# Kernel tuning notes

Measured on AMD Instinct MI355X. Metric: run time of the kernel, lower is better.

Reference implementation:

```python
import jax, jax.numpy as jnp
import numpy as np

IN_FEATURES = 8192
OUT_FEATURES = 8192
BATCH = 64


def setup_inputs() -> dict:
    key = jax.random.key(0)
    k_x, k_mu = jax.random.split(key)
    x = jax.random.normal(k_x, (BATCH, IN_FEATURES), dtype=jnp.float32)
    # torch init: mu = rand(in,1) * out_features; sigma = ones*10; amplitude = ones; bias = zeros
    mu = jax.random.uniform(k_mu, (IN_FEATURES, 1), dtype=jnp.float32) * OUT_FEATURES
    sigma = jnp.ones((IN_FEATURES, 1), dtype=jnp.float32) * 10.0
    amplitude = jnp.ones((IN_FEATURES, 1), dtype=jnp.float32)
    bias = jnp.zeros((OUT_FEATURES,), dtype=jnp.float32)
    return {"x": x, "mu": mu, "sigma": sigma, "amplitude": amplitude, "bias": bias}


def reference(x, mu, sigma, amplitude, bias):
    out_features = bias.shape[0]
    positions = jnp.arange(out_features, dtype=x.dtype)[None, :]  # [1, out]
    diff = positions - mu                                          # [in, out]
    weight = amplitude * jnp.exp(-(diff * diff) / (2.0 * sigma * sigma))  # [in, out]
    out = x @ weight                                               # [B, out]
    return jax.nn.relu(out + bias)
```

## Files before the change

### kernel.cpp

```cpp
#include <hip/hip_runtime.h>

#define IN_F 8192
#define OUT_F 8192
#define BATCH 64
#define TQ 64
#define NTILE (OUT_F / TQ)
#define ROWS 16
#define PASS 2048
#define CH 64

__global__ __launch_bounds__(256) void transpose_x_kern(const float* __restrict__ x,
                                                        float* __restrict__ xT) {
    __shared__ float tile[64][65];
    const int i0 = blockIdx.x * 64;
    const int tid = threadIdx.x;
#pragma unroll
    for (int u = tid; u < 64 * 64; u += 256) {
        const int b = u >> 6;
        const int i = u & 63;
        tile[i][b] = x[b * IN_F + i0 + i];
    }
    __syncthreads();
#pragma unroll
    for (int u = tid; u < 64 * 64; u += 256) {
        const int i = u >> 6;
        const int b = u & 63;
        xT[(i0 + i) * 64 + b] = tile[i][b];
    }
}

__global__ __launch_bounds__(256, 2) void gauss_fc_kern(
    const float* __restrict__ x, const float* __restrict__ xT,
    const float4* __restrict__ mu4, const float4* __restrict__ sg4,
    const float* __restrict__ amp, const float* __restrict__ bias,
    float* __restrict__ out, const int use_xt) {

    __shared__ float4 list[PASS];
    __shared__ float wtile[CH][64];
    __shared__ float xtile[CH][ROWS];
    __shared__ int   cnt;

    const int tid = threadIdx.x;
    const int cc = (tid & 31) << 1;
    const int g = tid >> 5;
    const int g2 = g << 1;
    const int tile0 = blockIdx.x * TQ;
    const int row0 = blockIdx.y * ROWS;
    const float lo = (float)tile0;
    const float hi = (float)(tile0 + TQ - 1);

    float acc00 = 0.f, acc01 = 0.f, acc10 = 0.f, acc11 = 0.f;

    for (int base = 0; base < IN_F; base += PASS) {
        if (tid == 0) cnt = 0;
        __syncthreads();

        const int q_end = (base + PASS) >> 2;
        for (int q = (base >> 2) + tid; q < q_end; q += 256) {
            const float4 m4 = mu4[q];
            const float4 s4 = sg4[q];
            const float ms[4] = {m4.x, m4.y, m4.z, m4.w};
            const float ss[4] = {s4.x, s4.y, s4.z, s4.w};
#pragma unroll
            for (int e = 0; e < 4; ++e) {
                const float m = ms[e];
                const float s = ss[e];
                const float R = 5.0f * fabsf(s) + 1.0f;
                if (m >= lo - R && m <= hi + R) {
                    const int i = (q << 2) + e;
                    const int p = atomicAdd(&cnt, 1);
                    list[p] = make_float4(m, -0.72134752f / (s * s), amp[i],
                                          __int_as_float(i));
                }
            }
        }
        __syncthreads();
        const int n = cnt;

        for (int cb = 0; cb < n; cb += CH) {
            const int cn = min(CH, n - cb);

            for (int u = tid; u < (cn << 6); u += 256) {
                const int j = u >> 6;
                const int col = u & 63;
                const float4 e = list[cb + j];
                const float d = (float)(tile0 + col) - e.x;
                wtile[j][col] = e.z * exp2f(e.y * d * d);
            }
            {
                const int ci = tid >> 2;
                const int rq = (tid & 3) << 2;
                if (ci < cn) {
                    const int i = __float_as_int(list[cb + ci].w);
                    if (use_xt) {
                        *(float4*)&xtile[ci][rq] = *(const float4*)&xT[i * 64 + row0 + rq];
                    } else {
                        xtile[ci][rq + 0] = x[(size_t)(row0 + rq + 0) * IN_F + i];
                        xtile[ci][rq + 1] = x[(size_t)(row0 + rq + 1) * IN_F + i];
                        xtile[ci][rq + 2] = x[(size_t)(row0 + rq + 2) * IN_F + i];
                        xtile[ci][rq + 3] = x[(size_t)(row0 + rq + 3) * IN_F + i];
                    }
                }
            }
            __syncthreads();

#pragma unroll 8
            for (int j = 0; j < cn; ++j) {
                const float2 wv = *(const float2*)&wtile[j][cc];
                const float2 xv = *(const float2*)&xtile[j][g2];
                acc00 += wv.x * xv.x;
                acc01 += wv.x * xv.y;
                acc10 += wv.y * xv.x;
                acc11 += wv.y * xv.y;
            }
            __syncthreads();
        }
    }

    const float b0 = bias[tile0 + cc];
    const float b1 = bias[tile0 + cc + 1];
    const int r0 = row0 + g2;
    float2 v0 = make_float2(fmaxf(acc00 + b0, 0.f), fmaxf(acc10 + b1, 0.f));
    float2 v1 = make_float2(fmaxf(acc01 + b0, 0.f), fmaxf(acc11 + b1, 0.f));
    *(float2*)&out[(size_t)r0 * OUT_F + tile0 + cc]       = v0;
    *(float2*)&out[(size_t)(r0 + 1) * OUT_F + tile0 + cc] = v1;
}

extern "C" void kernel_launch(void* const* d_in, const int* in_sizes, int n_in,
                              void* d_out, int out_size, void* d_ws, size_t ws_size,
                              hipStream_t stream) {
    const float* x     = (const float*)d_in[0];
    const float* mu    = (const float*)d_in[1];
    const float* sigma = (const float*)d_in[2];
    const float* amp   = (const float*)d_in[3];
    const float* bias  = (const float*)d_in[4];
    float* out = (float*)d_out;

    const size_t xt_bytes = (size_t)IN_F * BATCH * sizeof(float);
    const int use_xt = (ws_size >= xt_bytes) ? 1 : 0;
    float* xT = (float*)d_ws;

    if (use_xt) {
        transpose_x_kern<<<IN_F / 64, 256, 0, stream>>>(x, xT);
    }
    dim3 grid(NTILE, BATCH / ROWS);
    gauss_fc_kern<<<grid, 256, 0, stream>>>(x, xT,
                                            (const float4*)mu, (const float4*)sigma,
                                            amp, bias, out, use_xt);
}
```

Measured before the change: 86.62 us.

## Bin Gaussian inputs into per-tile candidate lists in a prep kernel

Previously every output-tile block scanned all 8192 mu/sigma entries and filtered them with shared-memory atomics. Now a prep kernel does that scan once: it computes each input's range of overlapping tiles and appends it to global per-tile lists, fused with the x transpose. The main kernel then loads its tile's list and the matching xT rows into shared memory up front and runs the weight-generation plus FMA loop. This removes the redundant per-block scans at the cost of a memset, global atomics and an extra launch. Lists are capped at 512 entries per tile, so any overflow beyond that cap is silently dropped.

```diff
diff --git a/kernel.cpp b/kernel.cpp
--- a/kernel.cpp
+++ b/kernel.cpp
@@ -6,27 +6,117 @@
 #define TQ 64
 #define NTILE (OUT_F / TQ)
 #define ROWS 16
+#define CH 64
+#define CAP 512
 #define PASS 2048
-#define CH 64
-
-__global__ __launch_bounds__(256) void transpose_x_kern(const float* __restrict__ x,
-                                                        float* __restrict__ xT) {
-    __shared__ float tile[64][65];
-    const int i0 = blockIdx.x * 64;
+
+#define XT_BYTES   ((size_t)IN_F * BATCH * sizeof(float))
+#define CNT_OFF    XT_BYTES
+#define LIST_OFF   (XT_BYTES + 1024)
+#define LIST_BYTES ((size_t)NTILE * CAP * sizeof(float4))
+#define WS_NEEDED  (LIST_OFF + LIST_BYTES)
+
+__global__ __launch_bounds__(256) void prep_kern(
+    const float* __restrict__ x, const float* __restrict__ mu,
+    const float* __restrict__ sigma, const float* __restrict__ amp,
+    float* __restrict__ xT, int* __restrict__ cnt, float4* __restrict__ list) {
     const int tid = threadIdx.x;
+    if (blockIdx.x < NTILE) {
+        __shared__ float tile[64][65];
+        const int i0 = blockIdx.x * 64;
 #pragma unroll
-    for (int u = tid; u < 64 * 64; u += 256) {
-        const int b = u >> 6;
-        const int i = u & 63;
-        tile[i][b] = x[b * IN_F + i0 + i];
-    }
+        for (int u = tid; u < 64 * 64; u += 256) {
+            const int b = u >> 6;
+            const int i = u & 63;
+            tile[i][b] = x[b * IN_F + i0 + i];
+        }
+        __syncthreads();
+#pragma unroll
+        for (int u = tid; u < 64 * 64; u += 256) {
+            const int i = u >> 6;
+            const int b = u & 63;
+            xT[(i0 + i) * 64 + b] = tile[i][b];
+        }
+    } else {
+        const int i = (blockIdx.x - NTILE) * 256 + tid;
+        const float m = mu[i];
+        const float s = sigma[i];
+        const float R = 5.0f * fabsf(s) + 1.0f;
+        int t0 = (int)ceilf((m - R - 63.0f) * (1.0f / 64.0f));
+        int t1 = (int)floorf((m + R) * (1.0f / 64.0f));
+        t0 = max(t0, 0);
+        t1 = min(t1, NTILE - 1);
+        const float4 e = make_float4(m, -0.72134752f / (s * s), amp[i],
+                                     __int_as_float(i));
+        for (int t = t0; t <= t1; ++t) {
+            const int p = atomicAdd(&cnt[t], 1);
+            if (p < CAP) list[(size_t)t * CAP + p] = e;
+        }
+    }
+}
+
+__global__ __launch_bounds__(256, 2) void gauss_main(
+    const float4* __restrict__ list, const int* __restrict__ cnt,
+    const float* __restrict__ xT, const float* __restrict__ bias,
+    float* __restrict__ out) {
+
+    __shared__ float4 lstage[CAP];
+    __shared__ float  xall[CAP][ROWS];
+    __shared__ float  wtile[CH][64];
+
+    const int tid = threadIdx.x;
+    const int cc = (tid & 31) << 1;
+    const int g = tid >> 5;
+    const int g2 = g << 1;
+    const int t = blockIdx.x;
+    const int tile0 = t * TQ;
+    const int row0 = blockIdx.y * ROWS;
+    const int n = min(cnt[t], CAP);
+    const float4* lp = list + (size_t)t * CAP;
+
+    for (int q = tid; q < n; q += 256) lstage[q] = lp[q];
     __syncthreads();
-#pragma unroll
-    for (int u = tid; u < 64 * 64; u += 256) {
-        const int i = u >> 6;
-        const int b = u & 63;
-        xT[(i0 + i) * 64 + b] = tile[i][b];
-    }
+
+    for (int u = tid; u < (n << 2); u += 256) {
+        const int ci = u >> 2;
+        const int rq = (u & 3) << 2;
+        const int i = __float_as_int(lstage[ci].w);
+        *(float4*)&xall[ci][rq] = *(const float4*)&xT[i * 64 + row0 + rq];
+    }
+
+    float acc00 = 0.f, acc01 = 0.f, acc10 = 0.f, acc11 = 0.f;
+
+    for (int cb = 0; cb < n; cb += CH) {
+        const int cn = min(CH, n - cb);
+
+        for (int u = tid; u < (cn << 6); u += 256) {
+            const int j = u >> 6;
+            const int col = u & 63;
+            const float4 e = lstage[cb + j];
+            const float d = (float)(tile0 + col) - e.x;
+            wtile[j][col] = e.z * exp2f(e.y * d * d);
+        }
+        __syncthreads();
+
+#pragma unroll 8
+        for (int j = 0; j < cn; ++j) {
+            const float2 wv = *(const float2*)&wtile[j][cc];
+            const float2 xv = *(const float2*)&xall[cb + j][g2];
+            acc00 += wv.x * xv.x;
+            acc01 += wv.x * xv.y;
+            acc10 += wv.y * xv.x;
+            acc11 += wv.y * xv.y;
+        }
+        __syncthreads();
+    }
+
+    const float b0 = bias[tile0 + cc];
+    const float b1 = bias[tile0 + cc + 1];
+    const int r0 = row0 + g2;
+    float2 v0 = make_float2(fmaxf(acc00 + b0, 0.f), fmaxf(acc10 + b1, 0.f));
+    float2 v1 = make_float2(fmaxf(acc01 + b0, 0.f), fmaxf(acc11 + b1, 0.f));
+    *(float2*)&out[(size_t)r0 * OUT_F + tile0 + cc]       = v0;
+    *(float2*)&out[(size_t)(r0 + 1) * OUT_F + tile0 + cc] = v1;
 }
 
 __global__ __launch_bounds__(256, 2) void gauss_fc_kern(
@@ -54,7 +144,6 @@
     for (int base = 0; base < IN_F; base += PASS) {
         if (tid == 0) cnt = 0;
         __syncthreads();
-
         const int q_end = (base + PASS) >> 2;
         for (int q = (base >> 2) + tid; q < q_end; q += 256) {
             const float4 m4 = mu4[q];
@@ -79,7 +168,6 @@
 
         for (int cb = 0; cb < n; cb += CH) {
             const int cn = min(CH, n - cb);
-
             for (int u = tid; u < (cn << 6); u += 256) {
                 const int j = u >> 6;
                 const int col = u & 63;
@@ -103,7 +191,6 @@
                 }
             }
             __syncthreads();
-
 #pragma unroll 8
             for (int j = 0; j < cn; ++j) {
                 const float2 wv = *(const float2*)&wtile[j][cc];
@@ -136,15 +223,19 @@
     const float* bias  = (const float*)d_in[4];
     float* out = (float*)d_out;
 
-    const size_t xt_bytes = (size_t)IN_F * BATCH * sizeof(float);
-    const int use_xt = (ws_size >= xt_bytes) ? 1 : 0;
-    float* xT = (float*)d_ws;
-
-    if (use_xt) {
-        transpose_x_kern<<<IN_F / 64, 256, 0, stream>>>(x, xT);
-    }
-    dim3 grid(NTILE, BATCH / ROWS);
-    gauss_fc_kern<<<grid, 256, 0, stream>>>(x, xT,
-                                            (const float4*)mu, (const float4*)sigma,
-                                            amp, bias, out, use_xt);
-}
+    if (ws_size >= WS_NEEDED) {
+        float*  xT   = (float*)d_ws;
+        int*    cnt  = (int*)((char*)d_ws + CNT_OFF);
+        float4* list = (float4*)((char*)d_ws + LIST_OFF);
+        hipMemsetAsync(cnt, 0, NTILE * sizeof(int), stream);
+        prep_kern<<<NTILE + IN_F / 256, 256, 0, stream>>>(x, mu, sigma, amp,
+                                                          xT, cnt, list);
+        dim3 grid(NTILE, BATCH / ROWS);
+        gauss_main<<<grid, 256, 0, stream>>>(list, cnt, xT, bias, out);
+    } else {
+        dim3 grid(NTILE, BATCH / ROWS);
+        gauss_fc_kern<<<grid, 256, 0, stream>>>(x, nullptr,
+                                                (const float4*)mu, (const float4*)sigma,
+                                                amp, bias, out, 0);
+    }
+}
```

Result: slower. 95.42 us (+10.2%).

## Drop x transpose kernel and use 512-thread blocks over 32 batch rows

Applied to the files above, without the earlier changes.

Removes the separate transpose pre-pass and gathers x columns directly from global memory inside the main kernel. Doubles threads per block to 512 and rows per block to 32, so each block covers half the batch and the mu/sigma scan and weight computation run half as often across the grid. Each scan pass now has one mu/sigma float4 per thread with no loop. The direct gather of x is strided, 8192 floats apart across rows, which may cost more than the old coalesced transposed reads. The grid halves to 256 blocks.

```diff
diff --git a/kernel.cpp b/kernel.cpp
--- a/kernel.cpp
+++ b/kernel.cpp
@@ -5,45 +5,25 @@
 #define BATCH 64
 #define TQ 64
 #define NTILE (OUT_F / TQ)
-#define ROWS 16
+#define ROWS 32
 #define PASS 2048
 #define CH 64
+#define NT 512
 
-__global__ __launch_bounds__(256) void transpose_x_kern(const float* __restrict__ x,
-                                                        float* __restrict__ xT) {
-    __shared__ float tile[64][65];
-    const int i0 = blockIdx.x * 64;
-    const int tid = threadIdx.x;
-#pragma unroll
-    for (int u = tid; u < 64 * 64; u += 256) {
-        const int b = u >> 6;
-        const int i = u & 63;
-        tile[i][b] = x[b * IN_F + i0 + i];
-    }
-    __syncthreads();
-#pragma unroll
-    for (int u = tid; u < 64 * 64; u += 256) {
-        const int i = u >> 6;
-        const int b = u & 63;
-        xT[(i0 + i) * 64 + b] = tile[i][b];
-    }
-}
-
-__global__ __launch_bounds__(256, 2) void gauss_fc_kern(
-    const float* __restrict__ x, const float* __restrict__ xT,
+__global__ __launch_bounds__(NT, 2) void gauss_fused(
+    const float* __restrict__ x,
     const float4* __restrict__ mu4, const float4* __restrict__ sg4,
     const float* __restrict__ amp, const float* __restrict__ bias,
-    float* __restrict__ out, const int use_xt) {
+    float* __restrict__ out) {
 
     __shared__ float4 list[PASS];
-    __shared__ float wtile[CH][64];
-    __shared__ float xtile[CH][ROWS];
-    __shared__ int   cnt;
+    __shared__ float  wtile[CH][64];
+    __shared__ float  xtile[CH][ROWS];
+    __shared__ int    cnt;
 
     const int tid = threadIdx.x;
     const int cc = (tid & 31) << 1;
-    const int g = tid >> 5;
-    const int g2 = g << 1;
+    const int g2 = (tid >> 5) << 1;
     const int tile0 = blockIdx.x * TQ;
     const int row0 = blockIdx.y * ROWS;
     const float lo = (float)tile0;
@@ -55,8 +35,8 @@
         if (tid == 0) cnt = 0;
         __syncthreads();
 
-        const int q_end = (base + PASS) >> 2;
-        for (int q = (base >> 2) + tid; q < q_end; q += 256) {
+        {
+            const int q = (base >> 2) + tid;
             const float4 m4 = mu4[q];
             const float4 s4 = sg4[q];
             const float ms[4] = {m4.x, m4.y, m4.z, m4.w};
@@ -80,27 +60,18 @@
         for (int cb = 0; cb < n; cb += CH) {
             const int cn = min(CH, n - cb);
 
-            for (int u = tid; u < (cn << 6); u += 256) {
+            for (int u = tid; u < (cn << 6); u += NT) {
                 const int j = u >> 6;
                 const int col = u & 63;
                 const float4 e = list[cb + j];
                 const float d = (float)(tile0 + col) - e.x;
                 wtile[j][col] = e.z * exp2f(e.y * d * d);
             }
-            {
-                const int ci = tid >> 2;
-                const int rq = (tid & 3) << 2;
-                if (ci < cn) {
-                    const int i = __float_as_int(list[cb + ci].w);
-                    if (use_xt) {
-                        *(float4*)&xtile[ci][rq] = *(const float4*)&xT[i * 64 + row0 + rq];
-                    } else {
-                        xtile[ci][rq + 0] = x[(size_t)(row0 + rq + 0) * IN_F + i];
-                        xtile[ci][rq + 1] = x[(size_t)(row0 + rq + 1) * IN_F + i];
-                        xtile[ci][rq + 2] = x[(size_t)(row0 + rq + 2) * IN_F + i];
-                        xtile[ci][rq + 3] = x[(size_t)(row0 + rq + 3) * IN_F + i];
-                    }
-                }
+            for (int u = tid; u < (cn << 5); u += NT) {
+                const int ci = u >> 5;
+                const int r = u & 31;
+                const int i = __float_as_int(list[cb + ci].w);
+                xtile[ci][r] = x[(size_t)(row0 + r) * IN_F + i];
             }
             __syncthreads();
 
@@ -135,16 +106,9 @@
     const float* amp   = (const float*)d_in[3];
     const float* bias  = (const float*)d_in[4];
     float* out = (float*)d_out;
+    (void)d_ws; (void)ws_size;
 
-    const size_t xt_bytes = (size_t)IN_F * BATCH * sizeof(float);
-    const int use_xt = (ws_size >= xt_bytes) ? 1 : 0;
-    float* xT = (float*)d_ws;
-
-    if (use_xt) {
-        transpose_x_kern<<<IN_F / 64, 256, 0, stream>>>(x, xT);
-    }
     dim3 grid(NTILE, BATCH / ROWS);
-    gauss_fc_kern<<<grid, 256, 0, stream>>>(x, xT,
-                                            (const float4*)mu, (const float4*)sigma,
-                                            amp, bias, out, use_xt);
+    gauss_fused<<<grid, NT, 0, stream>>>(x, (const float4*)mu, (const float4*)sigma,
+                                         amp, bias, out);
 }
```

After: 81.21 us. -6.3%, faster.
